# Kernel optimization log

Measured on AMD Instinct MI355X. Metric: run time of the kernel, lower is better.

Reference implementation:

```python
import jax, jax.numpy as jnp
import numpy as np

H = 1024
NS, NQ, S = 32, 64, 256
ADAPT_STEPS = 5


def _mlp_ln(x, W1, b1, W2, b2, g, be):
    # Linear -> ReLU -> Linear -> LayerNorm (dropout is identity in eval)
    h = jax.nn.relu(x @ W1 + b1) @ W2 + b2
    mu = h.mean(-1, keepdims=True)
    var = ((h - mu) ** 2).mean(-1, keepdims=True)
    return g * (h - mu) / jnp.sqrt(var + 1e-5) + be


def setup_inputs() -> dict:
    key = jax.random.key(0)
    ks = jax.random.split(key, 16)
    d = {}
    d['support_embeddings'] = jax.random.normal(ks[0], (NS, S, H), jnp.float32)
    d['query_embeddings'] = jax.random.normal(ks[1], (NQ, S, H), jnp.float32)
    d['support_labels'] = jax.random.randint(ks[2], (NS, S), 0, 3)
    w = lambda k, fi, fo: jax.random.normal(k, (fi, fo), jnp.float32) * (1.0 / np.sqrt(fi))
    # aspect_aware encoder
    d['aw_W1'] = w(ks[3], H, H); d['aw_b1'] = jnp.zeros((H,), jnp.float32)
    d['aw_W2'] = w(ks[4], H, H); d['aw_b2'] = jnp.zeros((H,), jnp.float32)
    d['aw_g'] = jnp.ones((H,), jnp.float32); d['aw_be'] = jnp.zeros((H,), jnp.float32)
    # aspect_contrastive encoder
    d['ct_W1'] = w(ks[5], H, H); d['ct_b1'] = jnp.zeros((H,), jnp.float32)
    d['ct_W2'] = w(ks[6], H, H); d['ct_b2'] = jnp.zeros((H,), jnp.float32)
    d['ct_g'] = jnp.ones((H,), jnp.float32); d['ct_be'] = jnp.zeros((H,), jnp.float32)
    # adaptation net (randomly-initialized 2-layer MLP in the torch code)
    d['ad_W1'] = w(ks[7], H, H); d['ad_b1'] = jnp.zeros((H,), jnp.float32)
    d['ad_W2'] = w(ks[8], H, H); d['ad_b2'] = jnp.zeros((H,), jnp.float32)
    # meta classifier
    d['cl_W1'] = w(ks[9], 2 * H, H); d['cl_b1'] = jnp.zeros((H,), jnp.float32)
    d['cl_W2'] = w(ks[10], H, 64); d['cl_b2'] = jnp.zeros((64,), jnp.float32)
    d['cl_W3'] = w(ks[11], 64, 3); d['cl_b3'] = jnp.zeros((3,), jnp.float32)
    return d


def reference(support_embeddings, query_embeddings, support_labels,
              aw_W1, aw_b1, aw_W2, aw_b2, aw_g, aw_be,
              ct_W1, ct_b1, ct_W2, ct_b2, ct_g, ct_be,
              ad_W1, ad_b1, ad_W2, ad_b2,
              cl_W1, cl_b1, cl_W2, cl_b2, cl_W3, cl_b3):
    # --- encode support set, build per-sentence aspect prototypes ---
    aw_s = _mlp_ln(support_embeddings, aw_W1, aw_b1, aw_W2, aw_b2, aw_g, aw_be)  # [NS,S,H]
    mask = (support_labels > 0).astype(aw_s.dtype)[..., None]                    # [NS,S,1]
    cnt = jnp.maximum(mask.sum(axis=1), 1.0)                                     # [NS,1]
    protos = (aw_s * mask).sum(axis=1) / cnt                                     # [NS,H] masked mean
    pn = protos / jnp.maximum(jnp.linalg.norm(protos, axis=-1, keepdims=True), 1e-8)

    # --- meta-adaptation: fused over all (query, token) pairs, 5 steps ---
    adapted = query_embeddings
    for _ in range(ADAPT_STEPS):
        qn = adapted / jnp.maximum(jnp.linalg.norm(adapted, axis=-1, keepdims=True), 1e-8)
        sims = jnp.einsum('qsh,ph->qsp', qn, pn)           # cosine similarities
        wts = jax.nn.softmax(sims, axis=-1)
        infl = jnp.einsum('qsp,ph->qsh', wts, protos)      # prototype influence
        adapted = jax.nn.relu((adapted + infl) @ ad_W1 + ad_b1) @ ad_W2 + ad_b2

    # --- classify adapted query tokens ---
    q_aw = _mlp_ln(adapted, aw_W1, aw_b1, aw_W2, aw_b2, aw_g, aw_be)
    q_ct = _mlp_ln(adapted, ct_W1, ct_b1, ct_W2, ct_b2, ct_g, ct_be)
    comb = jnp.concatenate([q_aw, q_ct], axis=-1)          # [NQ,S,2H]
    h = jax.nn.relu(comb @ cl_W1 + cl_b1)
    h = jax.nn.relu(h @ cl_W2 + cl_b2)
    preds = h @ cl_W3 + cl_b3                              # [NQ,S,3]
    return preds
```

## Files before the change

### kernel.cpp

```cpp
#include <hip/hip_runtime.h>
#include <hip/hip_bf16.h>

#define H 1024
#define NS 32
#define SS 256
#define T_Q 16384
#define M_S 8192

typedef __hip_bfloat16 bf16;
typedef short short8 __attribute__((ext_vector_type(8)));
typedef float floatx4 __attribute__((ext_vector_type(4)));

__device__ __forceinline__ float ldf(const bf16& v) { return __bfloat162float(v); }

__device__ __forceinline__ void split2(float v, bf16& h, bf16& l) {
  h = __float2bfloat16(v);
  l = __float2bfloat16(v - __bfloat162float(h));
}

__device__ __forceinline__ void gl2lds16(const void* g, void* l) {
  __builtin_amdgcn_global_load_lds(
      (const __attribute__((address_space(1))) unsigned int*)g,
      (__attribute__((address_space(3))) unsigned int*)l, 16, 0, 0);
}

__global__ __launch_bounds__(256) void conv_split(const float* __restrict__ in,
                                                  bf16* __restrict__ oh,
                                                  bf16* __restrict__ ol, int n)
{
  int i = blockIdx.x * 256 + threadIdx.x;
  if (i < n) { bf16 h, l; split2(in[i], h, l); oh[i] = h; ol[i] = l; }
}

__global__ __launch_bounds__(256) void transpose_split(
    const float* __restrict__ W, bf16* __restrict__ Wh, bf16* __restrict__ Wl,
    int K, int N)
{
  __shared__ float t[32][33];
  int n0 = blockIdx.x * 32, k0 = blockIdx.y * 32;
  int tx = threadIdx.x & 31, ty = threadIdx.x >> 5;
#pragma unroll
  for (int i = 0; i < 32; i += 8)
    t[ty + i][tx] = W[(size_t)(k0 + ty + i) * N + (n0 + tx)];
  __syncthreads();
#pragma unroll
  for (int i = 0; i < 32; i += 8) {
    bf16 h, l; split2(t[tx][ty + i], h, l);
    size_t o = (size_t)(n0 + ty + i) * K + (k0 + tx);
    Wh[o] = h;
    if (Wl) Wl[o] = l;
  }
}

template<bool RELU>
__global__ __launch_bounds__(256) void gemm3(
    const bf16* __restrict__ A0h, const bf16* __restrict__ A0l,
    const bf16* __restrict__ A1h, const bf16* __restrict__ A1l,
    const bf16* __restrict__ Wh,  const bf16* __restrict__ Wl,
    const float* __restrict__ bias,
    bf16* __restrict__ Ch, bf16* __restrict__ Cl,
    int M, int N, int K0, int Ktot)
{
  __shared__ bf16 Ash[128 * 32];
  __shared__ bf16 Asl[128 * 32];
  __shared__ bf16 Bsh[128 * 32];
  __shared__ bf16 Bsl[128 * 32];
  const int tid = threadIdx.x;
  const int w = tid >> 6, l = tid & 63;
  const int bm0 = blockIdx.x * 128, bn0 = blockIdx.y * 128;
  const int wr = (w >> 1) * 64, wc = (w & 1) * 64;
  const int m16 = l & 15, quad = l >> 4;
  const bool haveWl = (Wl != nullptr);

  floatx4 acc[4][4];
#pragma unroll
  for (int i = 0; i < 4; i++)
#pragma unroll
    for (int j = 0; j < 4; j++) { acc[i][j][0]=0.f; acc[i][j][1]=0.f; acc[i][j][2]=0.f; acc[i][j][3]=0.f; }

  const int ar = w * 16 + (l >> 2);
  const int ac = (l & 3) * 8;

  for (int k0 = 0; k0 < Ktot; k0 += 32) {
    const bf16 *Abh, *Abl;
    if (k0 < K0) { Abh = A0h + k0; Abl = A0l + k0; }
    else         { Abh = A1h + (k0 - K0); Abl = A1l + (k0 - K0); }
    gl2lds16(Abh + (size_t)(bm0 + ar) * H + ac,      &Ash[w * 512]);
    gl2lds16(Abh + (size_t)(bm0 + 64 + ar) * H + ac, &Ash[2048 + w * 512]);
    gl2lds16(Abl + (size_t)(bm0 + ar) * H + ac,      &Asl[w * 512]);
    gl2lds16(Abl + (size_t)(bm0 + 64 + ar) * H + ac, &Asl[2048 + w * 512]);
    const bf16* Bbh = Wh + k0;
    gl2lds16(Bbh + (size_t)(bn0 + ar) * Ktot + ac,      &Bsh[w * 512]);
    gl2lds16(Bbh + (size_t)(bn0 + 64 + ar) * Ktot + ac, &Bsh[2048 + w * 512]);
    if (haveWl) {
      const bf16* Bbl = Wl + k0;
      gl2lds16(Bbl + (size_t)(bn0 + ar) * Ktot + ac,      &Bsl[w * 512]);
      gl2lds16(Bbl + (size_t)(bn0 + 64 + ar) * Ktot + ac, &Bsl[2048 + w * 512]);
    }
    __syncthreads();

    short8 afh[4], afl[4], bfh[4], bfl[4];
#pragma unroll
    for (int mt = 0; mt < 4; mt++) {
      afh[mt] = *(const short8*)&Ash[(wr + mt * 16 + m16) * 32 + quad * 8];
      afl[mt] = *(const short8*)&Asl[(wr + mt * 16 + m16) * 32 + quad * 8];
    }
#pragma unroll
    for (int nt = 0; nt < 4; nt++)
      bfh[nt] = *(const short8*)&Bsh[(wc + nt * 16 + m16) * 32 + quad * 8];
    if (haveWl) {
#pragma unroll
      for (int nt = 0; nt < 4; nt++)
        bfl[nt] = *(const short8*)&Bsl[(wc + nt * 16 + m16) * 32 + quad * 8];
    }
#pragma unroll
    for (int mt = 0; mt < 4; mt++)
#pragma unroll
      for (int nt = 0; nt < 4; nt++) {
        acc[mt][nt] = __builtin_amdgcn_mfma_f32_16x16x32_bf16(afh[mt], bfh[nt], acc[mt][nt], 0, 0, 0);
        acc[mt][nt] = __builtin_amdgcn_mfma_f32_16x16x32_bf16(afl[mt], bfh[nt], acc[mt][nt], 0, 0, 0);
      }
    if (haveWl) {
#pragma unroll
      for (int mt = 0; mt < 4; mt++)
#pragma unroll
        for (int nt = 0; nt < 4; nt++)
          acc[mt][nt] = __builtin_amdgcn_mfma_f32_16x16x32_bf16(afh[mt], bfl[nt], acc[mt][nt], 0, 0, 0);
    }
    __syncthreads();
  }

#pragma unroll
  for (int mt = 0; mt < 4; mt++) {
#pragma unroll
    for (int nt = 0; nt < 4; nt++) {
      int row0 = bm0 + wr + mt * 16 + quad * 4;
      int col  = bn0 + wc + nt * 16 + m16;
      float bv = bias ? bias[col] : 0.f;
#pragma unroll
      for (int r = 0; r < 4; r++) {
        float v = acc[mt][nt][r] + bv;
        if (RELU) v = fmaxf(v, 0.f);
        bf16 h, lo; split2(v, h, lo);
        size_t o = (size_t)(row0 + r) * N + col;
        Ch[o] = h; Cl[o] = lo;
      }
    }
  }
}

__global__ __launch_bounds__(256) void ln_pair(
    bf16* __restrict__ hh, bf16* __restrict__ hl,
    const float* __restrict__ g, const float* __restrict__ be)
{
  int row = blockIdx.x;
  bf16* ph = hh + (size_t)row * H;
  bf16* pl = hl + (size_t)row * H;
  int tid = threadIdx.x;
  float v[4];
  float s = 0.f, sq = 0.f;
#pragma unroll
  for (int j = 0; j < 4; j++) {
    int hi = tid + 256 * j;
    v[j] = ldf(ph[hi]) + ldf(pl[hi]);
    s += v[j]; sq += v[j] * v[j];
  }
  __shared__ float rs[256], rq[256];
  rs[tid] = s; rq[tid] = sq; __syncthreads();
  for (int o = 128; o; o >>= 1) {
    if (tid < o) { rs[tid] += rs[tid + o]; rq[tid] += rq[tid + o]; }
    __syncthreads();
  }
  float mu   = rs[0] * (1.0f / H);
  float var  = rq[0] * (1.0f / H) - mu * mu;
  float rstd = rsqrtf(var + 1e-5f);
#pragma unroll
  for (int j = 0; j < 4; j++) {
    int hi = tid + 256 * j;
    bf16 h, l; split2(g[hi] * (v[j] - mu) * rstd + be[hi], h, l);
    ph[hi] = h; pl[hi] = l;
  }
}

__global__ __launch_bounds__(256) void proto_kernel(
    const bf16* __restrict__ eh, const bf16* __restrict__ el,
    const int* __restrict__ labels, float* __restrict__ protos_out)
{
  int p = blockIdx.x;
  int tid = threadIdx.x;
  __shared__ unsigned char lbl[SS];
  lbl[tid] = (labels[p * SS + tid] > 0) ? 1 : 0;
  __syncthreads();
  float acc[4] = {0.f, 0.f, 0.f, 0.f};
  int cnt = 0;
  const bf16* bh = eh + (size_t)p * SS * H;
  const bf16* bl = el + (size_t)p * SS * H;
  for (int s = 0; s < SS; s++) {
    if (lbl[s]) {
      cnt++;
      const bf16* rh = bh + (size_t)s * H;
      const bf16* rl = bl + (size_t)s * H;
#pragma unroll
      for (int j = 0; j < 4; j++)
        acc[j] += ldf(rh[tid + 256 * j]) + ldf(rl[tid + 256 * j]);
    }
  }
  float ic = 1.0f / fmaxf((float)cnt, 1.0f);
#pragma unroll
  for (int j = 0; j < 4; j++) protos_out[p * H + tid + 256 * j] = acc[j] * ic;
}

__global__ __launch_bounds__(256) void pn_kernel(
    const float* __restrict__ protos, bf16* __restrict__ pnh, bf16* __restrict__ pnl)
{
  int p = blockIdx.x;
  int tid = threadIdx.x;
  __shared__ float red[256];
  float v[4];
  float sq = 0.f;
#pragma unroll
  for (int j = 0; j < 4; j++) { v[j] = protos[p * H + tid + 256 * j]; sq += v[j] * v[j]; }
  red[tid] = sq; __syncthreads();
  for (int o = 128; o; o >>= 1) {
    if (tid < o) red[tid] += red[tid + o];
    __syncthreads();
  }
  float inv = 1.0f / fmaxf(sqrtf(red[0]), 1e-8f);
#pragma unroll
  for (int j = 0; j < 4; j++) {
    bf16 h, l; split2(v[j] * inv, h, l);
    pnh[p * H + tid + 256 * j] = h;
    pnl[p * H + tid + 256 * j] = l;
  }
}

__global__ __launch_bounds__(256) void rownorm_pair(
    const bf16* __restrict__ hh, const bf16* __restrict__ hl, float* __restrict__ rn)
{
  int row = blockIdx.x;
  int tid = threadIdx.x;
  const bf16* ph = hh + (size_t)row * H;
  const bf16* pl = hl + (size_t)row * H;
  float s = 0.f;
#pragma unroll
  for (int j = 0; j < 4; j++) {
    float v = ldf(ph[tid + 256 * j]) + ldf(pl[tid + 256 * j]);
    s += v * v;
  }
  __shared__ float rs[256];
  rs[tid] = s; __syncthreads();
  for (int o = 128; o; o >>= 1) {
    if (tid < o) rs[tid] += rs[tid + o];
    __syncthreads();
  }
  if (tid == 0) rn[row] = 1.0f / fmaxf(sqrtf(rs[0]), 1e-8f);
}

__global__ __launch_bounds__(256) void sims_mfma(
    const bf16* __restrict__ Ah, const bf16* __restrict__ Al,
    const bf16* __restrict__ Bh, const bf16* __restrict__ Bl,
    float* __restrict__ sims)
{
  __shared__ bf16 AsH[64 * 32];
  __shared__ bf16 AsL[64 * 32];
  __shared__ bf16 BsH[32 * 32];
  __shared__ bf16 BsL[32 * 32];
  const int tid = threadIdx.x;
  const int w = tid >> 6, l = tid & 63;
  const int bm0 = blockIdx.x * 64;
  const int m16 = l & 15, quad = l >> 4;
  const int sr = l >> 2;
  const int sc = (l & 3) * 8;

  floatx4 acc[2];
#pragma unroll
  for (int nt = 0; nt < 2; nt++) { acc[nt][0]=0.f; acc[nt][1]=0.f; acc[nt][2]=0.f; acc[nt][3]=0.f; }

  for (int k0 = 0; k0 < H; k0 += 32) {
    gl2lds16(Ah + (size_t)(bm0 + w * 16 + sr) * H + k0 + sc, &AsH[w * 512]);
    gl2lds16(Al + (size_t)(bm0 + w * 16 + sr) * H + k0 + sc, &AsL[w * 512]);
    if (w < 2) gl2lds16(Bh + (size_t)(w * 16 + sr) * H + k0 + sc, &BsH[w * 512]);
    else       gl2lds16(Bl + (size_t)((w - 2) * 16 + sr) * H + k0 + sc, &BsL[(w - 2) * 512]);
    __syncthreads();

    short8 ah  = *(const short8*)&AsH[(w * 16 + m16) * 32 + quad * 8];
    short8 al8 = *(const short8*)&AsL[(w * 16 + m16) * 32 + quad * 8];
#pragma unroll
    for (int nt = 0; nt < 2; nt++) {
      short8 bh  = *(const short8*)&BsH[(nt * 16 + m16) * 32 + quad * 8];
      short8 bl8 = *(const short8*)&BsL[(nt * 16 + m16) * 32 + quad * 8];
      acc[nt] = __builtin_amdgcn_mfma_f32_16x16x32_bf16(ah,  bh,  acc[nt], 0, 0, 0);
      acc[nt] = __builtin_amdgcn_mfma_f32_16x16x32_bf16(al8, bh,  acc[nt], 0, 0, 0);
      acc[nt] = __builtin_amdgcn_mfma_f32_16x16x32_bf16(ah,  bl8, acc[nt], 0, 0, 0);
    }
    __syncthreads();
  }

#pragma unroll
  for (int nt = 0; nt < 2; nt++) {
    int col  = nt * 16 + m16;
    int row0 = bm0 + w * 16 + quad * 4;
#pragma unroll
    for (int r = 0; r < 4; r++)
      sims[(size_t)(row0 + r) * 32 + col] = acc[nt][r];
  }
}

__global__ __launch_bounds__(256) void softmax32(
    const float* __restrict__ sims, const float* __restrict__ rn,
    float* __restrict__ wts)
{
  int t = blockIdx.x * 8 + (threadIdx.x >> 5);
  int p = threadIdx.x & 31;
  float s = sims[(size_t)t * 32 + p] * rn[t];
  float m = s;
#pragma unroll
  for (int o = 16; o; o >>= 1) m = fmaxf(m, __shfl_xor(m, o, 64));
  float e = __expf(s - m);
  float sum = e;
#pragma unroll
  for (int o = 16; o; o >>= 1) sum += __shfl_xor(sum, o, 64);
  wts[(size_t)t * 32 + p] = e / sum;
}

__global__ __launch_bounds__(256) void infl16(
    const bf16* __restrict__ ah, const bf16* __restrict__ al,
    const float* __restrict__ wts, const float* __restrict__ protos,
    bf16* __restrict__ oh, bf16* __restrict__ ol)
{
  int t0 = blockIdx.x * 16;
  int tid = threadIdx.x;
  __shared__ float wl[16][32];
  for (int i = tid; i < 512; i += 256)
    wl[i >> 5][i & 31] = wts[(size_t)(t0 + (i >> 5)) * 32 + (i & 31)];
  __syncthreads();
  int c0 = tid * 4;
  float acc[16][4];
#pragma unroll
  for (int tk = 0; tk < 16; tk++) {
    const bf16* rh = ah + (size_t)(t0 + tk) * H + c0;
    const bf16* rl = al + (size_t)(t0 + tk) * H + c0;
#pragma unroll
    for (int j = 0; j < 4; j++) acc[tk][j] = ldf(rh[j]) + ldf(rl[j]);
  }
  for (int p = 0; p < 32; p++) {
    float4 pv = *(const float4*)&protos[p * H + c0];
#pragma unroll
    for (int tk = 0; tk < 16; tk++) {
      float w = wl[tk][p];
      acc[tk][0] += w * pv.x; acc[tk][1] += w * pv.y;
      acc[tk][2] += w * pv.z; acc[tk][3] += w * pv.w;
    }
  }
#pragma unroll
  for (int tk = 0; tk < 16; tk++) {
    bf16* wh = oh + (size_t)(t0 + tk) * H + c0;
    bf16* wo = ol + (size_t)(t0 + tk) * H + c0;
#pragma unroll
    for (int j = 0; j < 4; j++) { bf16 h, lo; split2(acc[tk][j], h, lo); wh[j] = h; wo[j] = lo; }
  }
}

__global__ __launch_bounds__(256) void gemm_small(
    const bf16* __restrict__ Ah, const bf16* __restrict__ Al,
    const float* __restrict__ W, const float* __restrict__ bias,
    float* __restrict__ C, int M, int N, int K)
{
  const int BK = 16;
  __shared__ float As[BK][64];
  __shared__ float Bs[BK][64];
  int tid = threadIdx.x;
  int tx = tid & 15, ty = tid >> 4;
  int bn0 = blockIdx.x * 64;
  int bm0 = blockIdx.y * 64;
  float acc[4][4] = {};
  int am = tid >> 2, ak = (tid & 3) * 4;
  int bk = tid >> 4, bn = (tid & 15) * 4;
  const bf16* Aph = Ah + (size_t)(bm0 + am) * K + ak;
  const bf16* Apl = Al + (size_t)(bm0 + am) * K + ak;
  const float* Wptr = W + (size_t)bk * N + bn0 + bn;
  for (int k0 = 0; k0 < K; k0 += BK) {
#pragma unroll
    for (int c = 0; c < 4; c++) As[ak + c][am] = ldf(Aph[c]) + ldf(Apl[c]);
#pragma unroll
    for (int c = 0; c < 4; c++) Bs[bk][bn + c] = Wptr[c];
    __syncthreads();
#pragma unroll
    for (int k = 0; k < BK; k++) {
      float a[4], b[4];
#pragma unroll
      for (int i = 0; i < 4; i++) a[i] = As[k][ty * 4 + i];
#pragma unroll
      for (int j = 0; j < 4; j++) b[j] = Bs[k][tx * 4 + j];
#pragma unroll
      for (int i = 0; i < 4; i++)
#pragma unroll
        for (int j = 0; j < 4; j++)
          acc[i][j] += a[i] * b[j];
    }
    __syncthreads();
    Aph += BK; Apl += BK;
    Wptr += (size_t)BK * N;
  }
#pragma unroll
  for (int i = 0; i < 4; i++) {
    float* Crow = C + (size_t)(bm0 + ty * 4 + i) * N + bn0;
#pragma unroll
    for (int j = 0; j < 4; j++) {
      int n = tx * 4 + j;
      Crow[n] = fmaxf(acc[i][j] + bias[bn0 + n], 0.f);
    }
  }
}

__global__ __launch_bounds__(256) void FewShotABSALearner_46935402610855_kernel(
    const float* __restrict__ h2, const float* __restrict__ W3,
    const float* __restrict__ b3, float* __restrict__ out,
    int t0, int nElem, int out_size)
{
  int idx = blockIdx.x * 256 + threadIdx.x;
  if (idx >= nElem) return;
  int t = idx / 3, c = idx - t * 3;
  float acc = b3[c];
  const float* hr = h2 + (size_t)t * 64;
#pragma unroll
  for (int k = 0; k < 64; k++) acc += hr[k] * W3[k * 3 + c];
  int oi = t0 * 3 + idx;
  if (oi < out_size) out[oi] = acc;
}

extern "C" void kernel_launch(void* const* d_in, const int* in_sizes, int n_in,
                              void* d_out, int out_size, void* d_ws, size_t ws_size,
                              hipStream_t stream)
{
  (void)in_sizes; (void)n_in;
  const float* sup   = (const float*)d_in[0];
  const float* qry   = (const float*)d_in[1];
  const int*   lab   = (const int*)d_in[2];
  const float *aw_W1 = (const float*)d_in[3],  *aw_b1 = (const float*)d_in[4];
  const float *aw_W2 = (const float*)d_in[5],  *aw_b2 = (const float*)d_in[6];
  const float *aw_g  = (const float*)d_in[7],  *aw_be = (const float*)d_in[8];
  const float *ct_W1 = (const float*)d_in[9],  *ct_b1 = (const float*)d_in[10];
  const float *ct_W2 = (const float*)d_in[11], *ct_b2 = (const float*)d_in[12];
  const float *ct_g  = (const float*)d_in[13], *ct_be = (const float*)d_in[14];
  const float *ad_W1 = (const float*)d_in[15], *ad_b1 = (const float*)d_in[16];
  const float *ad_W2 = (const float*)d_in[17], *ad_b2 = (const float*)d_in[18];
  const float *cl_W1 = (const float*)d_in[19], *cl_b1 = (const float*)d_in[20];
  const float *cl_W2 = (const float*)d_in[21], *cl_b2 = (const float*)d_in[22];
  const float *cl_W3 = (const float*)d_in[23], *cl_b3 = (const float*)d_in[24];
  float* out = (float*)d_out;

  const size_t MB = 1 << 20;
  int C; bool clLo = true;
  if      (ws_size >= (size_t)239403008) C = 16384;
  else if (ws_size >= (size_t)136609792) C = 8192;
  else if (ws_size >= (size_t)85213184)  C = 4096;
  else if (ws_size >= (size_t)59514880)  C = 2048;
  else if (ws_size >= (size_t)46665728)  C = 1024;
  else { C = 1024; clLo = false; }
  const int Cs = (C < M_S) ? C : M_S;
  const size_t actB = (size_t)C * H * sizeof(bf16);

  char* ws = (char*)d_ws;
  size_t off = 0;
  auto nxt = [&](size_t b) { char* p = ws + off; off += b; return p; };
  bf16* sqw[12];
  for (int i = 0; i < 12; i++) sqw[i] = (bf16*)nxt(2 * MB);
  bf16 *aw1h = sqw[0], *aw1l = sqw[1], *aw2h = sqw[2],  *aw2l = sqw[3];
  bf16 *ct1h = sqw[4], *ct1l = sqw[5], *ct2h = sqw[6],  *ct2l = sqw[7];
  bf16 *ad1h = sqw[8], *ad1l = sqw[9], *ad2h = sqw[10], *ad2l = sqw[11];
  bf16* clW1h = (bf16*)nxt(4 * MB);
  bf16* clW1l = clLo ? (bf16*)nxt(4 * MB) : nullptr;
  float* protos = (float*)nxt(NS * H * 4);
  bf16*  pnh    = (bf16*)nxt(NS * H * 2);
  bf16*  pnl    = (bf16*)nxt(NS * H * 2);
  char*  ub     = nxt((size_t)C * 256);
  float* h2c   = (float*)ub;
  float* simsb = (float*)ub;
  float* wtsb  = (float*)(ub + (size_t)C * 128);
  float* rn    = (float*)nxt((size_t)C * 4);
  bf16 *R0h = (bf16*)nxt(actB), *R0l = (bf16*)nxt(actB);
  bf16 *R1h = (bf16*)nxt(actB), *R1l = (bf16*)nxt(actB);
  bf16 *R2h = (bf16*)nxt(actB), *R2l = (bf16*)nxt(actB);

  dim3 blk(256);
  dim3 tg(32, 32);
  dim3 gg(C / 128, H / 128);
  dim3 gs(Cs / 128, H / 128);

  transpose_split<<<tg, blk, 0, stream>>>(aw_W1, aw1h, aw1l, H, H);
  transpose_split<<<tg, blk, 0, stream>>>(aw_W2, aw2h, aw2l, H, H);
  transpose_split<<<tg, blk, 0, stream>>>(ct_W1, ct1h, ct1l, H, H);
  transpose_split<<<tg, blk, 0, stream>>>(ct_W2, ct2h, ct2l, H, H);
  transpose_split<<<tg, blk, 0, stream>>>(ad_W1, ad1h, ad1l, H, H);
  transpose_split<<<tg, blk, 0, stream>>>(ad_W2, ad2h, ad2l, H, H);
  transpose_split<<<dim3(32, 64), blk, 0, stream>>>(cl_W1, clW1h, clW1l, 2 * H, H);

  for (int sc = 0; sc < M_S / Cs; sc++) {
    conv_split<<<(Cs * H) / 256, blk, 0, stream>>>(sup + (size_t)sc * Cs * H, R0h, R0l, Cs * H);
    gemm3<true ><<<gs, blk, 0, stream>>>(R0h, R0l, R0h, R0l, aw1h, aw1l, aw_b1, R1h, R1l, Cs, H, H, H);
    gemm3<false><<<gs, blk, 0, stream>>>(R1h, R1l, R1h, R1l, aw2h, aw2l, aw_b2, R2h, R2l, Cs, H, H, H);
    ln_pair<<<Cs, blk, 0, stream>>>(R2h, R2l, aw_g, aw_be);
    proto_kernel<<<Cs / SS, blk, 0, stream>>>(R2h, R2l, lab + sc * Cs,
                                              protos + (size_t)sc * (Cs / SS) * H);
  }
  pn_kernel<<<NS, blk, 0, stream>>>(protos, pnh, pnl);

  for (int qc = 0; qc < T_Q / C; qc++) {
    const float* q0 = qry + (size_t)qc * C * H;
    conv_split<<<(C * H) / 256, blk, 0, stream>>>(q0, R2h, R2l, C * H);
    for (int it = 0; it < 5; it++) {
      rownorm_pair<<<C, blk, 0, stream>>>(R2h, R2l, rn);
      sims_mfma<<<C / 64, blk, 0, stream>>>(R2h, R2l, pnh, pnl, simsb);
      softmax32<<<C / 8, blk, 0, stream>>>(simsb, rn, wtsb);
      infl16<<<C / 16, blk, 0, stream>>>(R2h, R2l, wtsb, protos, R0h, R0l);
      gemm3<true ><<<gg, blk, 0, stream>>>(R0h, R0l, R0h, R0l, ad1h, ad1l, ad_b1, R1h, R1l, C, H, H, H);
      gemm3<false><<<gg, blk, 0, stream>>>(R1h, R1l, R1h, R1l, ad2h, ad2l, ad_b2, R2h, R2l, C, H, H, H);
    }
    gemm3<true ><<<gg, blk, 0, stream>>>(R2h, R2l, R2h, R2l, aw1h, aw1l, aw_b1, R0h, R0l, C, H, H, H);
    gemm3<false><<<gg, blk, 0, stream>>>(R0h, R0l, R0h, R0l, aw2h, aw2l, aw_b2, R1h, R1l, C, H, H, H);
    ln_pair<<<C, blk, 0, stream>>>(R1h, R1l, aw_g, aw_be);
    gemm3<true ><<<gg, blk, 0, stream>>>(R2h, R2l, R2h, R2l, ct1h, ct1l, ct_b1, R0h, R0l, C, H, H, H);
    gemm3<false><<<gg, blk, 0, stream>>>(R0h, R0l, R0h, R0l, ct2h, ct2l, ct_b2, R2h, R2l, C, H, H, H);
    ln_pair<<<C, blk, 0, stream>>>(R2h, R2l, ct_g, ct_be);
    gemm3<true ><<<gg, blk, 0, stream>>>(R1h, R1l, R2h, R2l, clW1h, clW1l, cl_b1, R0h, R0l, C, H, H, 2 * H);
    gemm_small<<<dim3(1, C / 64), blk, 0, stream>>>(R0h, R0l, cl_W2, cl_b2, h2c, C, 64, H);
    FewShotABSALearner_46935402610855_kernel<<<(C * 3 + 255) / 256, blk, 0, stream>>>(
        h2c, cl_W3, cl_b3, out, qc * C, C * 3, out_size);
  }
}
```

Measured before the change: 2.793 ms.

## Rewrite split-bf16 GEMM with triple-buffered LDS pipeline and 256x128 tiles

Replaces the synchronous split-bf16 GEMM with a 512-thread kernel that computes 256x128 output tiles. Global-to-LDS loads are triple-buffered and kept two k-steps ahead, with explicit vmcnt waits in place of full syncthreads. It also uses s_setprio around the MFMA bursts and compiles the low-weight path as a template parameter. The aim is to hide load latency and reuse B tiles across more rows, at the cost of more LDS per block and lower occupancy. Correctness now depends on the hand-counted vmcnt values matching the number of issued loads.

```diff
diff --git a/kernel.cpp b/kernel.cpp
--- a/kernel.cpp
+++ b/kernel.cpp
@@ -24,6 +24,8 @@
       (__attribute__((address_space(3))) unsigned int*)l, 16, 0, 0);
 }
 
+__device__ __forceinline__ short8 ld8s(const bf16* p) { return *(const short8*)p; }
+
 __global__ __launch_bounds__(256) void conv_split(const float* __restrict__ in,
                                                   bf16* __restrict__ oh,
                                                   bf16* __restrict__ ol, int n)
@@ -52,8 +54,8 @@
   }
 }
 
-template<bool RELU>
-__global__ __launch_bounds__(256) void gemm3(
+template<bool RELU, bool HASWL>
+__global__ __launch_bounds__(512) void gemm3p(
     const bf16* __restrict__ A0h, const bf16* __restrict__ A0l,
     const bf16* __restrict__ A1h, const bf16* __restrict__ A1l,
     const bf16* __restrict__ Wh,  const bf16* __restrict__ Wl,
@@ -61,16 +63,15 @@
     bf16* __restrict__ Ch, bf16* __restrict__ Cl,
     int M, int N, int K0, int Ktot)
 {
-  __shared__ bf16 Ash[128 * 32];
-  __shared__ bf16 Asl[128 * 32];
-  __shared__ bf16 Bsh[128 * 32];
-  __shared__ bf16 Bsl[128 * 32];
+  (void)M;
+  __shared__ __align__(16) bf16 lds[3 * 24576];
   const int tid = threadIdx.x;
   const int w = tid >> 6, l = tid & 63;
-  const int bm0 = blockIdx.x * 128, bn0 = blockIdx.y * 128;
-  const int wr = (w >> 1) * 64, wc = (w & 1) * 64;
+  const int bm0 = blockIdx.x * 256, bn0 = blockIdx.y * 128;
+  const int wr = w >> 1, wn = w & 1;
   const int m16 = l & 15, quad = l >> 4;
-  const bool haveWl = (Wl != nullptr);
+  const int srow = l & 15;
+  const int scol = (l >> 4) * 8;
 
   floatx4 acc[4][4];
 #pragma unroll
@@ -78,68 +79,96 @@
 #pragma unroll
     for (int j = 0; j < 4; j++) { acc[i][j][0]=0.f; acc[i][j][1]=0.f; acc[i][j][2]=0.f; acc[i][j][3]=0.f; }
 
-  const int ar = w * 16 + (l >> 2);
-  const int ac = (l & 3) * 8;
-
-  for (int k0 = 0; k0 < Ktot; k0 += 32) {
-    const bf16 *Abh, *Abl;
-    if (k0 < K0) { Abh = A0h + k0; Abl = A0l + k0; }
-    else         { Abh = A1h + (k0 - K0); Abl = A1l + (k0 - K0); }
-    gl2lds16(Abh + (size_t)(bm0 + ar) * H + ac,      &Ash[w * 512]);
-    gl2lds16(Abh + (size_t)(bm0 + 64 + ar) * H + ac, &Ash[2048 + w * 512]);
-    gl2lds16(Abl + (size_t)(bm0 + ar) * H + ac,      &Asl[w * 512]);
-    gl2lds16(Abl + (size_t)(bm0 + 64 + ar) * H + ac, &Asl[2048 + w * 512]);
-    const bf16* Bbh = Wh + k0;
-    gl2lds16(Bbh + (size_t)(bn0 + ar) * Ktot + ac,      &Bsh[w * 512]);
-    gl2lds16(Bbh + (size_t)(bn0 + 64 + ar) * Ktot + ac, &Bsh[2048 + w * 512]);
-    if (haveWl) {
-      const bf16* Bbl = Wl + k0;
-      gl2lds16(Bbl + (size_t)(bn0 + ar) * Ktot + ac,      &Bsl[w * 512]);
-      gl2lds16(Bbl + (size_t)(bn0 + 64 + ar) * Ktot + ac, &Bsl[2048 + w * 512]);
-    }
-    __syncthreads();
-
-    short8 afh[4], afl[4], bfh[4], bfl[4];
-#pragma unroll
-    for (int mt = 0; mt < 4; mt++) {
-      afh[mt] = *(const short8*)&Ash[(wr + mt * 16 + m16) * 32 + quad * 8];
-      afl[mt] = *(const short8*)&Asl[(wr + mt * 16 + m16) * 32 + quad * 8];
-    }
-#pragma unroll
-    for (int nt = 0; nt < 4; nt++)
-      bfh[nt] = *(const short8*)&Bsh[(wc + nt * 16 + m16) * 32 + quad * 8];
-    if (haveWl) {
-#pragma unroll
-      for (int nt = 0; nt < 4; nt++)
-        bfl[nt] = *(const short8*)&Bsl[(wc + nt * 16 + m16) * 32 + quad * 8];
-    }
-#pragma unroll
-    for (int mt = 0; mt < 4; mt++)
-#pragma unroll
-      for (int nt = 0; nt < 4; nt++) {
-        acc[mt][nt] = __builtin_amdgcn_mfma_f32_16x16x32_bf16(afh[mt], bfh[nt], acc[mt][nt], 0, 0, 0);
-        acc[mt][nt] = __builtin_amdgcn_mfma_f32_16x16x32_bf16(afl[mt], bfh[nt], acc[mt][nt], 0, 0, 0);
-      }
-    if (haveWl) {
-#pragma unroll
-      for (int mt = 0; mt < 4; mt++)
-#pragma unroll
-        for (int nt = 0; nt < 4; nt++)
-          acc[mt][nt] = __builtin_amdgcn_mfma_f32_16x16x32_bf16(afh[mt], bfl[nt], acc[mt][nt], 0, 0, 0);
-    }
-    __syncthreads();
-  }
-
-#pragma unroll
-  for (int mt = 0; mt < 4; mt++) {
-#pragma unroll
-    for (int nt = 0; nt < 4; nt++) {
-      int row0 = bm0 + wr + mt * 16 + quad * 4;
-      int col  = bn0 + wc + nt * 16 + m16;
+  const size_t raA0 = (size_t)(bm0 + (2 * w)     * 16 + srow) * H + scol;
+  const size_t raA1 = (size_t)(bm0 + (2 * w + 1) * 16 + srow) * H + scol;
+  const size_t raB  = (size_t)(bn0 + w * 16 + srow) * Ktot + scol;
+  const int nT = Ktot >> 5;
+
+  auto stage = [&](int t) {
+    const int k0 = t << 5;
+    const bf16 *Abh, *Abl; int ke;
+    if (k0 < K0) { Abh = A0h; Abl = A0l; ke = k0; }
+    else         { Abh = A1h; Abl = A1l; ke = k0 - K0; }
+    bf16* buf = lds + (t % 3) * 24576;
+    gl2lds16(Abh + raA0 + ke, buf + (2 * w)     * 512);
+    gl2lds16(Abh + raA1 + ke, buf + (2 * w + 1) * 512);
+    gl2lds16(Abl + raA0 + ke, buf + 8192 + (2 * w)     * 512);
+    gl2lds16(Abl + raA1 + ke, buf + 8192 + (2 * w + 1) * 512);
+    gl2lds16(Wh + raB + k0, buf + 16384 + w * 512);
+    if (HASWL) gl2lds16(Wl + raB + k0, buf + 20480 + w * 512);
+  };
+
+  stage(0);
+  if (nT > 1) stage(1);
+
+  const int la = l * 8;
+  for (int t = 0; t < nT; ++t) {
+    const bf16* buf = lds + (t % 3) * 24576;
+    if (t + 2 < nT) {
+      stage(t + 2);
+      if (HASWL) asm volatile("s_waitcnt vmcnt(12)" ::: "memory");
+      else       asm volatile("s_waitcnt vmcnt(10)" ::: "memory");
+    } else if (t + 1 < nT) {
+      if (HASWL) asm volatile("s_waitcnt vmcnt(6)" ::: "memory");
+      else       asm volatile("s_waitcnt vmcnt(5)" ::: "memory");
+    } else {
+      asm volatile("s_waitcnt vmcnt(0)" ::: "memory");
+    }
+    __builtin_amdgcn_s_barrier();
+
+    const bf16* bA  = buf + (wr * 4) * 512 + la;
+    const bf16* bAl = bA + 8192;
+    const bf16* bB  = buf + 16384 + (wn * 4) * 512 + la;
+    const bf16* bBl = bB + 4096;
+
+    short8 bh[4], bl8[4];
+#pragma unroll
+    for (int ni = 0; ni < 4; ni++) bh[ni] = ld8s(bB + ni * 512);
+    if (HASWL) {
+#pragma unroll
+      for (int ni = 0; ni < 4; ni++) bl8[ni] = ld8s(bBl + ni * 512);
+    }
+
+#define MM3(MI, AH, AL)                                                                            \
+    _Pragma("unroll")                                                                              \
+    for (int ni = 0; ni < 4; ni++) {                                                               \
+      acc[MI][ni] = __builtin_amdgcn_mfma_f32_16x16x32_bf16(AH, bh[ni],  acc[MI][ni], 0, 0, 0);    \
+      acc[MI][ni] = __builtin_amdgcn_mfma_f32_16x16x32_bf16(AL, bh[ni],  acc[MI][ni], 0, 0, 0);    \
+      if (HASWL)                                                                                   \
+        acc[MI][ni] = __builtin_amdgcn_mfma_f32_16x16x32_bf16(AH, bl8[ni], acc[MI][ni], 0, 0, 0);  \
+    }
+
+    {
+      short8 a0h = ld8s(bA),          a1h = ld8s(bA + 512);
+      short8 a0l = ld8s(bAl),         a1l = ld8s(bAl + 512);
+      __builtin_amdgcn_s_setprio(1);
+      MM3(0, a0h, a0l)
+      MM3(1, a1h, a1l)
+      __builtin_amdgcn_s_setprio(0);
+    }
+    __builtin_amdgcn_s_barrier();
+    {
+      short8 a2h = ld8s(bA + 1024),   a3h = ld8s(bA + 1536);
+      short8 a2l = ld8s(bAl + 1024),  a3l = ld8s(bAl + 1536);
+      __builtin_amdgcn_s_setprio(1);
+      MM3(2, a2h, a2l)
+      MM3(3, a3h, a3l)
+      __builtin_amdgcn_s_setprio(0);
+    }
+    __builtin_amdgcn_s_barrier();
+#undef MM3
+  }
+
+#pragma unroll
+  for (int mi = 0; mi < 4; mi++) {
+#pragma unroll
+    for (int ni = 0; ni < 4; ni++) {
+      int row0 = bm0 + wr * 64 + mi * 16 + quad * 4;
+      int col  = bn0 + wn * 64 + ni * 16 + m16;
       float bv = bias ? bias[col] : 0.f;
 #pragma unroll
       for (int r = 0; r < 4; r++) {
-        float v = acc[mt][nt][r] + bv;
+        float v = acc[mi][ni][r] + bv;
         if (RELU) v = fmaxf(v, 0.f);
         bf16 h, lo; split2(v, h, lo);
         size_t o = (size_t)(row0 + r) * N + col;
@@ -484,9 +513,10 @@
   bf16 *R2h = (bf16*)nxt(actB), *R2l = (bf16*)nxt(actB);
 
   dim3 blk(256);
+  dim3 blk2(512);
   dim3 tg(32, 32);
-  dim3 gg(C / 128, H / 128);
-  dim3 gs(Cs / 128, H / 128);
+  dim3 gg2(C / 256, H / 128);
+  dim3 gs2(Cs / 256, H / 128);
 
   transpose_split<<<tg, blk, 0, stream>>>(aw_W1, aw1h, aw1l, H, H);
   transpose_split<<<tg, blk, 0, stream>>>(aw_W2, aw2h, aw2l, H, H);
@@ -498,8 +528,8 @@
 
   for (int sc = 0; sc < M_S / Cs; sc++) {
     conv_split<<<(Cs * H) / 256, blk, 0, stream>>>(sup + (size_t)sc * Cs * H, R0h, R0l, Cs * H);
-    gemm3<true ><<<gs, blk, 0, stream>>>(R0h, R0l, R0h, R0l, aw1h, aw1l, aw_b1, R1h, R1l, Cs, H, H, H);
-    gemm3<false><<<gs, blk, 0, stream>>>(R1h, R1l, R1h, R1l, aw2h, aw2l, aw_b2, R2h, R2l, Cs, H, H, H);
+    gemm3p<true , true><<<gs2, blk2, 0, stream>>>(R0h, R0l, R0h, R0l, aw1h, aw1l, aw_b1, R1h, R1l, Cs, H, H, H);
+    gemm3p<false, true><<<gs2, blk2, 0, stream>>>(R1h, R1l, R1h, R1l, aw2h, aw2l, aw_b2, R2h, R2l, Cs, H, H, H);
     ln_pair<<<Cs, blk, 0, stream>>>(R2h, R2l, aw_g, aw_be);
     proto_kernel<<<Cs / SS, blk, 0, stream>>>(R2h, R2l, lab + sc * Cs,
                                               protos + (size_t)sc * (Cs / SS) * H);
@@ -514,16 +544,19 @@
       sims_mfma<<<C / 64, blk, 0, stream>>>(R2h, R2l, pnh, pnl, simsb);
       softmax32<<<C / 8, blk, 0, stream>>>(simsb, rn, wtsb);
       infl16<<<C / 16, blk, 0, stream>>>(R2h, R2l, wtsb, protos, R0h, R0l);
-      gemm3<true ><<<gg, blk, 0, stream>>>(R0h, R0l, R0h, R0l, ad1h, ad1l, ad_b1, R1h, R1l, C, H, H, H);
-      gemm3<false><<<gg, blk, 0, stream>>>(R1h, R1l, R1h, R1l, ad2h, ad2l, ad_b2, R2h, R2l, C, H, H, H);
-    }
-    gemm3<true ><<<gg, blk, 0, stream>>>(R2h, R2l, R2h, R2l, aw1h, aw1l, aw_b1, R0h, R0l, C, H, H, H);
-    gemm3<false><<<gg, blk, 0, stream>>>(R0h, R0l, R0h, R0l, aw2h, aw2l, aw_b2, R1h, R1l, C, H, H, H);
+      gemm3p<true , true><<<gg2, blk2, 0, stream>>>(R0h, R0l, R0h, R0l, ad1h, ad1l, ad_b1, R1h, R1l, C, H, H, H);
+      gemm3p<false, true><<<gg2, blk2, 0, stream>>>(R1h, R1l, R1h, R1l, ad2h, ad2l, ad_b2, R2h, R2l, C, H, H, H);
+    }
+    gemm3p<true , true><<<gg2, blk2, 0, stream>>>(R2h, R2l, R2h, R2l, aw1h, aw1l, aw_b1, R0h, R0l, C, H, H, H);
+    gemm3p<false, true><<<gg2, blk2, 0, stream>>>(R0h, R0l, R0h, R0l, aw2h, aw2l, aw_b2, R1h, R1l, C, H, H, H);
     ln_pair<<<C, blk, 0, stream>>>(R1h, R1l, aw_g, aw_be);
-    gemm3<true ><<<gg, blk, 0, stream>>>(R2h, R2l, R2h, R2l, ct1h, ct1l, ct_b1, R0h, R0l, C, H, H, H);
-    gemm3<false><<<gg, blk, 0, stream>>>(R0h, R0l, R0h, R0l, ct2h, ct2l, ct_b2, R2h, R2l, C, H, H, H);
+    gemm3p<true , true><<<gg2, blk2, 0, stream>>>(R2h, R2l, R2h, R2l, ct1h, ct1l, ct_b1, R0h, R0l, C, H, H, H);
+    gemm3p<false, true><<<gg2, blk2, 0, stream>>>(R0h, R0l, R0h, R0l, ct2h, ct2l, ct_b2, R2h, R2l, C, H, H, H);
     ln_pair<<<C, blk, 0, stream>>>(R2h, R2l, ct_g, ct_be);
-    gemm3<true ><<<gg, blk, 0, stream>>>(R1h, R1l, R2h, R2l, clW1h, clW1l, cl_b1, R0h, R0l, C, H, H, 2 * H);
+    if (clLo)
+      gemm3p<true, true ><<<gg2, blk2, 0, stream>>>(R1h, R1l, R2h, R2l, clW1h, clW1l, cl_b1, R0h, R0l, C, H, H, 2 * H);
+    else
+      gemm3p<true, false><<<gg2, blk2, 0, stream>>>(R1h, R1l, R2h, R2l, clW1h, nullptr, cl_b1, R0h, R0l, C, H, H, 2 * H);
     gemm_small<<<dim3(1, C / 64), blk, 0, stream>>>(R0h, R0l, cl_W2, cl_b2, h2c, C, 64, H);
     FewShotABSALearner_46935402610855_kernel<<<(C * 3 + 255) / 256, blk, 0, stream>>>(
         h2c, cl_W3, cl_b3, out, qc * C, C * 3, out_size);
```

Measured after the change: 2.740 ms. Within noise of the previous version (-1.9%).
